# Optimization experiments

Hardware: AMD Instinct MI355X
Metric: run time of the kernel (lower is better)

## Reference

```python
import jax, jax.numpy as jnp
import numpy as np


def setup_inputs() -> dict:
    key = jax.random.key(0)
    k1, = jax.random.split(key, 1)
    b, l, h, w, c = 2, 16, 16, 16, 32
    inputs = jax.random.normal(k1, (b, l, h, w, c), dtype=jnp.float32)
    gamma = jnp.ones((1,), dtype=jnp.float32)
    return {"inputs": inputs, "gamma": gamma}


def reference(inputs, gamma):
    b, l, h, w, c = inputs.shape
    n = l * h * w
    # torch: x = permute->view gives [b, c, n]; here keep [b, n, c] (same memory layout of values)
    xr = inputs.reshape(b, n, c)
    # scores[b,i,j] = sum_c x[b,c,i] * x[b,c,j]
    scores = jnp.einsum('bic,bjc->bij', xr, xr)
    attn = jax.nn.softmax(scores, axis=-1)  # softmax over j (dim=-1)
    # out[b,c,j] = sum_i x[b,c,i] * attn[b,i,j]  ->  [b, n, c] layout
    out = jnp.einsum('bic,bij->bjc', xr, attn)
    out = out.reshape(b, l, h, w, c)
    return out * gamma + inputs
```

## Files before the change

### kernel.cpp

```cpp
#include <hip/hip_runtime.h>


typedef _Float16 half8 __attribute__((ext_vector_type(8)));
typedef _Float16 half4v __attribute__((ext_vector_type(4)));
typedef _Float16 half2v __attribute__((ext_vector_type(2)));
typedef float float4v __attribute__((ext_vector_type(4)));
typedef int int4v __attribute__((ext_vector_type(4)));

#define NN 4096
#define CC 32
#define L2E 1.44269504f
#define SHIFT 48.0f

__global__ __launch_bounds__(256) void k_convert(const float* __restrict__ x,
                                                 _Float16* __restrict__ xf,
                                                 _Float16* __restrict__ xt) {
    const int t = blockIdx.x * 256 + threadIdx.x;
    const int n  = t & 4095;
    const int cg = (t >> 12) & 7;
    const int b  = t >> 15;
    const int row = (b << 12) | n;
    const float4* src = (const float4*)(x + (size_t)row * CC + cg * 4);
    float4 v = *src;
    _Float16 h0 = (_Float16)v.x, h1 = (_Float16)v.y, h2 = (_Float16)v.z, h3 = (_Float16)v.w;
    *(half4v*)(xf + (size_t)row * CC + cg * 4) = (half4v){h0, h1, h2, h3};
    _Float16* xtb = xt + (size_t)b * CC * NN;
    xtb[(cg * 4 + 0) * NN + n] = h0;
    xtb[(cg * 4 + 1) * NN + n] = h1;
    xtb[(cg * 4 + 2) * NN + n] = h2;
    xtb[(cg * 4 + 3) * NN + n] = h3;
}

__global__ __launch_bounds__(512, 4) void k_pass1(const _Float16* __restrict__ xf,
                                                  float* __restrict__ c2out) {
    const int tid = threadIdx.x;
    const int wave = tid >> 6, lane = tid & 63;
    const int quad = lane >> 4, l15 = lane & 15;
    const int b = blockIdx.x >> 8;
    const int i0 = (blockIdx.x & 255) * 16;
    const _Float16* xb = xf + (size_t)b * NN * CC;

    const half8 afrag = *(const half8*)(xb + (size_t)(i0 + l15) * CC + quad * 8);
    const float4v zf = {0.f, 0.f, 0.f, 0.f};
    float z[4] = {0.f, 0.f, 0.f, 0.f};
    const float c2c = -SHIFT * L2E;

    const int jbase = wave * 512;
    half8 b0 = *(const half8*)(xb + (size_t)(jbase + l15) * CC + quad * 8);
    half8 b1 = *(const half8*)(xb + (size_t)(jbase + 16 + l15) * CC + quad * 8);
    half8 b2 = *(const half8*)(xb + (size_t)(jbase + 32 + l15) * CC + quad * 8);
    half8 b3 = *(const half8*)(xb + (size_t)(jbase + 48 + l15) * CC + quad * 8);

    for (int jt = 0; jt < 8; ++jt) {
        const int jn = jbase + ((jt + 1) & 7) * 64;
        half8 n0 = *(const half8*)(xb + (size_t)(jn + l15) * CC + quad * 8);
        half8 n1 = *(const half8*)(xb + (size_t)(jn + 16 + l15) * CC + quad * 8);
        half8 n2 = *(const half8*)(xb + (size_t)(jn + 32 + l15) * CC + quad * 8);
        half8 n3 = *(const half8*)(xb + (size_t)(jn + 48 + l15) * CC + quad * 8);

        float4v s0 = __builtin_amdgcn_mfma_f32_16x16x32_f16(afrag, b0, zf, 0, 0, 0);
        float4v s1 = __builtin_amdgcn_mfma_f32_16x16x32_f16(afrag, b1, zf, 0, 0, 0);
        float4v s2 = __builtin_amdgcn_mfma_f32_16x16x32_f16(afrag, b2, zf, 0, 0, 0);
        float4v s3 = __builtin_amdgcn_mfma_f32_16x16x32_f16(afrag, b3, zf, 0, 0, 0);
#pragma unroll
        for (int r = 0; r < 4; ++r) {
            z[r] += __builtin_amdgcn_exp2f(fmaf(s0[r], L2E, c2c));
            z[r] += __builtin_amdgcn_exp2f(fmaf(s1[r], L2E, c2c));
            z[r] += __builtin_amdgcn_exp2f(fmaf(s2[r], L2E, c2c));
            z[r] += __builtin_amdgcn_exp2f(fmaf(s3[r], L2E, c2c));
        }
        b0 = n0; b1 = n1; b2 = n2; b3 = n3;
    }
#pragma unroll
    for (int off = 1; off <= 8; off <<= 1) {
#pragma unroll
        for (int r = 0; r < 4; ++r) z[r] += __shfl_xor(z[r], off, 64);
    }
    __shared__ float zw[8][16];
    if (l15 == 0) {
#pragma unroll
        for (int r = 0; r < 4; ++r) zw[wave][quad * 4 + r] = z[r];
    }
    __syncthreads();
    if (tid < 16) {
        float zs = 0.f;
#pragma unroll
        for (int w = 0; w < 8; ++w) zs += zw[w][tid];
        c2out[b * NN + i0 + tid] = -(__builtin_amdgcn_logf(zs) + SHIFT * L2E);
    }
}

__global__ __launch_bounds__(512, 4) void k_pass2(const _Float16* __restrict__ xf,
                                                  const _Float16* __restrict__ xt,
                                                  const float* __restrict__ c2,
                                                  const float* __restrict__ x,
                                                  const float* __restrict__ gamma,
                                                  float* __restrict__ out) {
    const int tid = threadIdx.x;
    const int wave = tid >> 6, lane = tid & 63;
    const int quad = lane >> 4, l15 = lane & 15;
    const int b = blockIdx.x >> 8;
    const int j0 = (blockIdx.x & 255) * 16;
    const _Float16* xb  = xf + (size_t)b * NN * CC;
    const _Float16* xtb = xt + (size_t)b * CC * NN;
    const float* c2b = c2 + b * NN;

    __shared__ float red[8][16][32];

    const int addrLo = (((quad & 1) << 5) + l15) << 2;
    const int addrHi = addrLo + 64;
    const bool lo32 = (lane < 32);

    const half8 bjfrag = *(const half8*)(xb + (size_t)(j0 + l15) * CC + quad * 8);
    const float4v zf = {0.f, 0.f, 0.f, 0.f};
    float4v acc0 = zf, acc1 = zf;

    const int ibase = wave * 512;
    half8 a0  = *(const half8*)(xb + (size_t)(ibase + l15) * CC + quad * 8);
    half8 a1  = *(const half8*)(xb + (size_t)(ibase + 16 + l15) * CC + quad * 8);
    half8 xb0 = *(const half8*)(xtb + (size_t)l15 * NN + ibase + quad * 8);
    half8 xb1 = *(const half8*)(xtb + (size_t)(l15 + 16) * NN + ibase + quad * 8);
    float4v c20 = *(const float4v*)(c2b + ibase + quad * 4);
    float4v c21 = *(const float4v*)(c2b + ibase + 16 + quad * 4);

    for (int it = 0; it < 16; ++it) {
        const int inx = ibase + ((it + 1) & 15) * 32;
        half8 na0  = *(const half8*)(xb + (size_t)(inx + l15) * CC + quad * 8);
        half8 na1  = *(const half8*)(xb + (size_t)(inx + 16 + l15) * CC + quad * 8);
        half8 nxb0 = *(const half8*)(xtb + (size_t)l15 * NN + inx + quad * 8);
        half8 nxb1 = *(const half8*)(xtb + (size_t)(l15 + 16) * NN + inx + quad * 8);
        float4v nc20 = *(const float4v*)(c2b + inx + quad * 4);
        float4v nc21 = *(const float4v*)(c2b + inx + 16 + quad * 4);

        float4v s0 = __builtin_amdgcn_mfma_f32_16x16x32_f16(a0, bjfrag, zf, 0, 0, 0);
        float4v s1 = __builtin_amdgcn_mfma_f32_16x16x32_f16(a1, bjfrag, zf, 0, 0, 0);
        float4v e0, e1;
#pragma unroll
        for (int r = 0; r < 4; ++r) {
            e0[r] = __builtin_amdgcn_exp2f(fmaf(s0[r], L2E, c20[r]));
            e1[r] = __builtin_amdgcn_exp2f(fmaf(s1[r], L2E, c21[r]));
        }
        const int d0 = __builtin_bit_cast(int, (half2v)__builtin_amdgcn_cvt_pkrtz(e0[0], e0[1]));
        const int d1 = __builtin_bit_cast(int, (half2v)__builtin_amdgcn_cvt_pkrtz(e0[2], e0[3]));
        const int d2 = __builtin_bit_cast(int, (half2v)__builtin_amdgcn_cvt_pkrtz(e1[0], e1[1]));
        const int d3 = __builtin_bit_cast(int, (half2v)__builtin_amdgcn_cvt_pkrtz(e1[2], e1[3]));
        const int q0 = __builtin_amdgcn_ds_bpermute(addrLo, d0);
        const int q1 = __builtin_amdgcn_ds_bpermute(addrLo, d1);
        const int q2 = __builtin_amdgcn_ds_bpermute(addrHi, d0);
        const int q3 = __builtin_amdgcn_ds_bpermute(addrHi, d1);
        const int q4 = __builtin_amdgcn_ds_bpermute(addrLo, d2);
        const int q5 = __builtin_amdgcn_ds_bpermute(addrLo, d3);
        const int q6 = __builtin_amdgcn_ds_bpermute(addrHi, d2);
        const int q7 = __builtin_amdgcn_ds_bpermute(addrHi, d3);
        int4v ai;
        ai[0] = lo32 ? q0 : q4;
        ai[1] = lo32 ? q1 : q5;
        ai[2] = lo32 ? q2 : q6;
        ai[3] = lo32 ? q3 : q7;
        const half8 a2 = __builtin_bit_cast(half8, ai);

        acc0 = __builtin_amdgcn_mfma_f32_16x16x32_f16(a2, xb0, acc0, 0, 0, 0);
        acc1 = __builtin_amdgcn_mfma_f32_16x16x32_f16(a2, xb1, acc1, 0, 0, 0);

        a0 = na0; a1 = na1; xb0 = nxb0; xb1 = nxb1; c20 = nc20; c21 = nc21;
    }

#pragma unroll
    for (int r = 0; r < 4; ++r) {
        red[wave][quad * 4 + r][l15]      = acc0[r];
        red[wave][quad * 4 + r][l15 + 16] = acc1[r];
    }
    __syncthreads();
    {
        const int jj = tid >> 5, c = tid & 31;
        float s = 0.f;
#pragma unroll
        for (int w = 0; w < 8; ++w) s += red[w][jj][c];
        const float g = gamma[0];
        const size_t o = (size_t)(b * NN + j0 + jj) * CC + c;
        out[o] = fmaf(g, s, x[o]);
    }
}

extern "C" void kernel_launch(void* const* d_in, const int* in_sizes, int n_in,
                              void* d_out, int out_size, void* d_ws, size_t ws_size,
                              hipStream_t stream) {
    const float* x     = (const float*)d_in[0];
    const float* gamma = (const float*)d_in[1];
    float* out = (float*)d_out;

    _Float16* xf = (_Float16*)d_ws;
    _Float16* xt = xf + (size_t)2 * NN * CC;
    float*    c2 = (float*)(xt + (size_t)2 * CC * NN);

    k_convert<<<dim3(256), dim3(256), 0, stream>>>(x, xf, xt);
    k_pass1 <<<dim3(512), dim3(512), 0, stream>>>(xf, c2);
    k_pass2 <<<dim3(512), dim3(512), 0, stream>>>(xf, xt, c2, x, gamma, out);
}
```

Measured before the change: 93.24 us.

## Fuse convert, pass1 and pass2 into one cooperative kernel with grid syncs

Merges the three kernel launches into a single cooperative kernel that loops over tiles and separates the phases with grid-wide barriers. The goal is to remove launch overhead and inter-kernel gaps between the conversion, normalizer and output passes. In exchange it adds two grid.sync calls, host-side attribute and occupancy queries on every launch, and a grid capped by occupancy, which may mean fewer concurrent blocks per phase. The three-kernel path remains as a fallback.

```diff
diff --git a/kernel.cpp b/kernel.cpp
--- a/kernel.cpp
+++ b/kernel.cpp
@@ -1,5 +1,8 @@
 #include <hip/hip_runtime.h>
-
+#include <hip/hip_cooperative_groups.h>
+
+
+namespace cg = cooperative_groups;
 
 typedef _Float16 half8 __attribute__((ext_vector_type(8)));
 typedef _Float16 half4v __attribute__((ext_vector_type(4)));
@@ -12,32 +15,33 @@
 #define L2E 1.44269504f
 #define SHIFT 48.0f
 
-__global__ __launch_bounds__(256) void k_convert(const float* __restrict__ x,
-                                                 _Float16* __restrict__ xf,
-                                                 _Float16* __restrict__ xt) {
-    const int t = blockIdx.x * 256 + threadIdx.x;
+
+__device__ __forceinline__ void convert_body(int t, const float* __restrict__ x,
+                                             _Float16* __restrict__ xf,
+                                             _Float16* __restrict__ xt) {
     const int n  = t & 4095;
-    const int cg = (t >> 12) & 7;
+    const int cg_ = (t >> 12) & 7;
     const int b  = t >> 15;
     const int row = (b << 12) | n;
-    const float4* src = (const float4*)(x + (size_t)row * CC + cg * 4);
+    const float4* src = (const float4*)(x + (size_t)row * CC + cg_ * 4);
     float4 v = *src;
     _Float16 h0 = (_Float16)v.x, h1 = (_Float16)v.y, h2 = (_Float16)v.z, h3 = (_Float16)v.w;
-    *(half4v*)(xf + (size_t)row * CC + cg * 4) = (half4v){h0, h1, h2, h3};
+    *(half4v*)(xf + (size_t)row * CC + cg_ * 4) = (half4v){h0, h1, h2, h3};
     _Float16* xtb = xt + (size_t)b * CC * NN;
-    xtb[(cg * 4 + 0) * NN + n] = h0;
-    xtb[(cg * 4 + 1) * NN + n] = h1;
-    xtb[(cg * 4 + 2) * NN + n] = h2;
-    xtb[(cg * 4 + 3) * NN + n] = h3;
-}
-
-__global__ __launch_bounds__(512, 4) void k_pass1(const _Float16* __restrict__ xf,
-                                                  float* __restrict__ c2out) {
-    const int tid = threadIdx.x;
+    xtb[(cg_ * 4 + 0) * NN + n] = h0;
+    xtb[(cg_ * 4 + 1) * NN + n] = h1;
+    xtb[(cg_ * 4 + 2) * NN + n] = h2;
+    xtb[(cg_ * 4 + 3) * NN + n] = h3;
+}
+
+__device__ __forceinline__ void pass1_tile(int tile, int tid,
+                                           const _Float16* __restrict__ xf,
+                                           float* __restrict__ c2out,
+                                           float (*zw)[16]) {
     const int wave = tid >> 6, lane = tid & 63;
     const int quad = lane >> 4, l15 = lane & 15;
-    const int b = blockIdx.x >> 8;
-    const int i0 = (blockIdx.x & 255) * 16;
+    const int b = tile >> 8;
+    const int i0 = (tile & 255) * 16;
     const _Float16* xb = xf + (size_t)b * NN * CC;
 
     const half8 afrag = *(const half8*)(xb + (size_t)(i0 + l15) * CC + quad * 8);
@@ -76,7 +80,6 @@
 #pragma unroll
         for (int r = 0; r < 4; ++r) z[r] += __shfl_xor(z[r], off, 64);
     }
-    __shared__ float zw[8][16];
     if (l15 == 0) {
 #pragma unroll
         for (int r = 0; r < 4; ++r) zw[wave][quad * 4 + r] = z[r];
@@ -90,22 +93,21 @@
     }
 }
 
-__global__ __launch_bounds__(512, 4) void k_pass2(const _Float16* __restrict__ xf,
-                                                  const _Float16* __restrict__ xt,
-                                                  const float* __restrict__ c2,
-                                                  const float* __restrict__ x,
-                                                  const float* __restrict__ gamma,
-                                                  float* __restrict__ out) {
-    const int tid = threadIdx.x;
+__device__ __forceinline__ void pass2_tile(int tile, int tid,
+                                           const _Float16* __restrict__ xf,
+                                           const _Float16* __restrict__ xt,
+                                           const float* __restrict__ c2,
+                                           const float* __restrict__ x,
+                                           const float* __restrict__ gamma,
+                                           float* __restrict__ out,
+                                           float (*red)[16][32]) {
     const int wave = tid >> 6, lane = tid & 63;
     const int quad = lane >> 4, l15 = lane & 15;
-    const int b = blockIdx.x >> 8;
-    const int j0 = (blockIdx.x & 255) * 16;
+    const int b = tile >> 8;
+    const int j0 = (tile & 255) * 16;
     const _Float16* xb  = xf + (size_t)b * NN * CC;
     const _Float16* xtb = xt + (size_t)b * CC * NN;
     const float* c2b = c2 + b * NN;
-
-    __shared__ float red[8][16][32];
 
     const int addrLo = (((quad & 1) << 5) + l15) << 2;
     const int addrHi = addrLo + 64;
@@ -182,6 +184,60 @@
     }
 }
 
+
+__global__ __launch_bounds__(512, 4) void k_fused(const float* __restrict__ x,
+                                                  const float* __restrict__ gamma,
+                                                  _Float16* __restrict__ xf,
+                                                  _Float16* __restrict__ xt,
+                                                  float* __restrict__ c2,
+                                                  float* __restrict__ out) {
+    cg::grid_group grid = cg::this_grid();
+    const int tid = threadIdx.x;
+    const int nb = gridDim.x;
+
+    __shared__ float zw[8][16];
+    __shared__ float red[8][16][32];
+
+    for (int t = blockIdx.x * 512 + tid; t < 65536; t += nb * 512)
+        convert_body(t, x, xf, xt);
+    grid.sync();
+
+    for (int tile = blockIdx.x; tile < 512; tile += nb) {
+        pass1_tile(tile, tid, xf, c2, zw);
+        __syncthreads();
+    }
+    grid.sync();
+
+    for (int tile = blockIdx.x; tile < 512; tile += nb) {
+        pass2_tile(tile, tid, xf, xt, c2, x, gamma, out, red);
+        __syncthreads();
+    }
+}
+
+
+__global__ __launch_bounds__(256) void k_convert(const float* __restrict__ x,
+                                                 _Float16* __restrict__ xf,
+                                                 _Float16* __restrict__ xt) {
+    const int t = blockIdx.x * 256 + threadIdx.x;
+    convert_body(t, x, xf, xt);
+}
+
+__global__ __launch_bounds__(512, 4) void k_pass1(const _Float16* __restrict__ xf,
+                                                  float* __restrict__ c2out) {
+    __shared__ float zw[8][16];
+    pass1_tile(blockIdx.x, threadIdx.x, xf, c2out, zw);
+}
+
+__global__ __launch_bounds__(512, 4) void k_pass2(const _Float16* __restrict__ xf,
+                                                  const _Float16* __restrict__ xt,
+                                                  const float* __restrict__ c2,
+                                                  const float* __restrict__ x,
+                                                  const float* __restrict__ gamma,
+                                                  float* __restrict__ out) {
+    __shared__ float red[8][16][32];
+    pass2_tile(blockIdx.x, threadIdx.x, xf, xt, c2, x, gamma, out, red);
+}
+
 extern "C" void kernel_launch(void* const* d_in, const int* in_sizes, int n_in,
                               void* d_out, int out_size, void* d_ws, size_t ws_size,
                               hipStream_t stream) {
@@ -193,6 +249,20 @@
     _Float16* xt = xf + (size_t)2 * NN * CC;
     float*    c2 = (float*)(xt + (size_t)2 * CC * NN);
 
+    int coopAttr = 0;
+    (void)hipDeviceGetAttribute(&coopAttr, hipDeviceAttributeCooperativeLaunch, 0);
+    int occ = 0;
+    hipError_t oe = hipOccupancyMaxActiveBlocksPerMultiprocessor(&occ, k_fused, 512, 0);
+
+    if (coopAttr && oe == hipSuccess && occ > 0) {
+        int grid = occ * 256;
+        if (grid > 512) grid = 512;
+        void* args[] = {(void*)&x, (void*)&gamma, (void*)&xf, (void*)&xt, (void*)&c2, (void*)&out};
+        hipError_t le = hipLaunchCooperativeKernel(k_fused, dim3(grid), dim3(512),
+                                                   args, 0u, stream);
+        if (le == hipSuccess) return;
+    }
+
     k_convert<<<dim3(256), dim3(256), 0, stream>>>(x, xf, xt);
     k_pass1 <<<dim3(512), dim3(512), 0, stream>>>(xf, c2);
     k_pass2 <<<dim3(512), dim3(512), 0, stream>>>(xf, xt, c2, x, gamma, out);
```

Result: slower. 175.6 us (+88.3%).

## Process 32 query rows per block to reuse streamed key/value fragments

Applied to the files above, without the earlier changes.

Each block of both passes now handles 32 rows instead of 16, so each loaded j (or i) fragment feeds twice as many MFMAs. This halves redundant global/L2 traffic for streamed operands and the grid size. The trade-off is more registers per thread (launch bounds lowered to 2 blocks per CU), more shared memory for the reduction, and only 256 blocks, which may underfill the 256 CUs of the device.

```diff
diff --git a/kernel.cpp b/kernel.cpp
--- a/kernel.cpp
+++ b/kernel.cpp
@@ -31,18 +31,20 @@
     xtb[(cg * 4 + 3) * NN + n] = h3;
 }
 
-__global__ __launch_bounds__(512, 4) void k_pass1(const _Float16* __restrict__ xf,
+__global__ __launch_bounds__(512, 2) void k_pass1(const _Float16* __restrict__ xf,
                                                   float* __restrict__ c2out) {
     const int tid = threadIdx.x;
     const int wave = tid >> 6, lane = tid & 63;
     const int quad = lane >> 4, l15 = lane & 15;
-    const int b = blockIdx.x >> 8;
-    const int i0 = (blockIdx.x & 255) * 16;
+    const int b = blockIdx.x >> 7;
+    const int i0 = (blockIdx.x & 127) * 32;
     const _Float16* xb = xf + (size_t)b * NN * CC;
 
-    const half8 afrag = *(const half8*)(xb + (size_t)(i0 + l15) * CC + quad * 8);
+    const half8 af0 = *(const half8*)(xb + (size_t)(i0 + l15) * CC + quad * 8);
+    const half8 af1 = *(const half8*)(xb + (size_t)(i0 + 16 + l15) * CC + quad * 8);
     const float4v zf = {0.f, 0.f, 0.f, 0.f};
-    float z[4] = {0.f, 0.f, 0.f, 0.f};
+    float z0[4] = {0.f, 0.f, 0.f, 0.f};
+    float z1[4] = {0.f, 0.f, 0.f, 0.f};
     const float c2c = -SHIFT * L2E;
 
     const int jbase = wave * 512;
@@ -58,31 +60,45 @@
         half8 n2 = *(const half8*)(xb + (size_t)(jn + 32 + l15) * CC + quad * 8);
         half8 n3 = *(const half8*)(xb + (size_t)(jn + 48 + l15) * CC + quad * 8);
 
-        float4v s0 = __builtin_amdgcn_mfma_f32_16x16x32_f16(afrag, b0, zf, 0, 0, 0);
-        float4v s1 = __builtin_amdgcn_mfma_f32_16x16x32_f16(afrag, b1, zf, 0, 0, 0);
-        float4v s2 = __builtin_amdgcn_mfma_f32_16x16x32_f16(afrag, b2, zf, 0, 0, 0);
-        float4v s3 = __builtin_amdgcn_mfma_f32_16x16x32_f16(afrag, b3, zf, 0, 0, 0);
-#pragma unroll
-        for (int r = 0; r < 4; ++r) {
-            z[r] += __builtin_amdgcn_exp2f(fmaf(s0[r], L2E, c2c));
-            z[r] += __builtin_amdgcn_exp2f(fmaf(s1[r], L2E, c2c));
-            z[r] += __builtin_amdgcn_exp2f(fmaf(s2[r], L2E, c2c));
-            z[r] += __builtin_amdgcn_exp2f(fmaf(s3[r], L2E, c2c));
+        float4v s00 = __builtin_amdgcn_mfma_f32_16x16x32_f16(af0, b0, zf, 0, 0, 0);
+        float4v s01 = __builtin_amdgcn_mfma_f32_16x16x32_f16(af0, b1, zf, 0, 0, 0);
+        float4v s02 = __builtin_amdgcn_mfma_f32_16x16x32_f16(af0, b2, zf, 0, 0, 0);
+        float4v s03 = __builtin_amdgcn_mfma_f32_16x16x32_f16(af0, b3, zf, 0, 0, 0);
+        float4v s10 = __builtin_amdgcn_mfma_f32_16x16x32_f16(af1, b0, zf, 0, 0, 0);
+        float4v s11 = __builtin_amdgcn_mfma_f32_16x16x32_f16(af1, b1, zf, 0, 0, 0);
+        float4v s12 = __builtin_amdgcn_mfma_f32_16x16x32_f16(af1, b2, zf, 0, 0, 0);
+        float4v s13 = __builtin_amdgcn_mfma_f32_16x16x32_f16(af1, b3, zf, 0, 0, 0);
+#pragma unroll
+        for (int r = 0; r < 4; ++r) {
+            z0[r] += __builtin_amdgcn_exp2f(fmaf(s00[r], L2E, c2c));
+            z0[r] += __builtin_amdgcn_exp2f(fmaf(s01[r], L2E, c2c));
+            z0[r] += __builtin_amdgcn_exp2f(fmaf(s02[r], L2E, c2c));
+            z0[r] += __builtin_amdgcn_exp2f(fmaf(s03[r], L2E, c2c));
+            z1[r] += __builtin_amdgcn_exp2f(fmaf(s10[r], L2E, c2c));
+            z1[r] += __builtin_amdgcn_exp2f(fmaf(s11[r], L2E, c2c));
+            z1[r] += __builtin_amdgcn_exp2f(fmaf(s12[r], L2E, c2c));
+            z1[r] += __builtin_amdgcn_exp2f(fmaf(s13[r], L2E, c2c));
         }
         b0 = n0; b1 = n1; b2 = n2; b3 = n3;
     }
 #pragma unroll
     for (int off = 1; off <= 8; off <<= 1) {
 #pragma unroll
-        for (int r = 0; r < 4; ++r) z[r] += __shfl_xor(z[r], off, 64);
-    }
-    __shared__ float zw[8][16];
+        for (int r = 0; r < 4; ++r) {
+            z0[r] += __shfl_xor(z0[r], off, 64);
+            z1[r] += __shfl_xor(z1[r], off, 64);
+        }
+    }
+    __shared__ float zw[8][32];
     if (l15 == 0) {
 #pragma unroll
-        for (int r = 0; r < 4; ++r) zw[wave][quad * 4 + r] = z[r];
+        for (int r = 0; r < 4; ++r) {
+            zw[wave][quad * 4 + r]      = z0[r];
+            zw[wave][16 + quad * 4 + r] = z1[r];
+        }
     }
     __syncthreads();
-    if (tid < 16) {
+    if (tid < 32) {
         float zs = 0.f;
 #pragma unroll
         for (int w = 0; w < 8; ++w) zs += zw[w][tid];
@@ -90,7 +106,7 @@
     }
 }
 
-__global__ __launch_bounds__(512, 4) void k_pass2(const _Float16* __restrict__ xf,
+__global__ __launch_bounds__(512, 2) void k_pass2(const _Float16* __restrict__ xf,
                                                   const _Float16* __restrict__ xt,
                                                   const float* __restrict__ c2,
                                                   const float* __restrict__ x,
@@ -99,21 +115,22 @@
     const int tid = threadIdx.x;
     const int wave = tid >> 6, lane = tid & 63;
     const int quad = lane >> 4, l15 = lane & 15;
-    const int b = blockIdx.x >> 8;
-    const int j0 = (blockIdx.x & 255) * 16;
+    const int b = blockIdx.x >> 7;
+    const int j0 = (blockIdx.x & 127) * 32;
     const _Float16* xb  = xf + (size_t)b * NN * CC;
     const _Float16* xtb = xt + (size_t)b * CC * NN;
     const float* c2b = c2 + b * NN;
 
-    __shared__ float red[8][16][32];
+    __shared__ float red[8][32][32];
 
     const int addrLo = (((quad & 1) << 5) + l15) << 2;
     const int addrHi = addrLo + 64;
     const bool lo32 = (lane < 32);
 
-    const half8 bjfrag = *(const half8*)(xb + (size_t)(j0 + l15) * CC + quad * 8);
+    const half8 bj0 = *(const half8*)(xb + (size_t)(j0 + l15) * CC + quad * 8);
+    const half8 bj1 = *(const half8*)(xb + (size_t)(j0 + 16 + l15) * CC + quad * 8);
     const float4v zf = {0.f, 0.f, 0.f, 0.f};
-    float4v acc0 = zf, acc1 = zf;
+    float4v acc00 = zf, acc01 = zf, acc10 = zf, acc11 = zf;
 
     const int ibase = wave * 512;
     half8 a0  = *(const half8*)(xb + (size_t)(ibase + l15) * CC + quad * 8);
@@ -132,53 +149,86 @@
         float4v nc20 = *(const float4v*)(c2b + inx + quad * 4);
         float4v nc21 = *(const float4v*)(c2b + inx + 16 + quad * 4);
 
-        float4v s0 = __builtin_amdgcn_mfma_f32_16x16x32_f16(a0, bjfrag, zf, 0, 0, 0);
-        float4v s1 = __builtin_amdgcn_mfma_f32_16x16x32_f16(a1, bjfrag, zf, 0, 0, 0);
-        float4v e0, e1;
-#pragma unroll
-        for (int r = 0; r < 4; ++r) {
-            e0[r] = __builtin_amdgcn_exp2f(fmaf(s0[r], L2E, c20[r]));
-            e1[r] = __builtin_amdgcn_exp2f(fmaf(s1[r], L2E, c21[r]));
-        }
-        const int d0 = __builtin_bit_cast(int, (half2v)__builtin_amdgcn_cvt_pkrtz(e0[0], e0[1]));
-        const int d1 = __builtin_bit_cast(int, (half2v)__builtin_amdgcn_cvt_pkrtz(e0[2], e0[3]));
-        const int d2 = __builtin_bit_cast(int, (half2v)__builtin_amdgcn_cvt_pkrtz(e1[0], e1[1]));
-        const int d3 = __builtin_bit_cast(int, (half2v)__builtin_amdgcn_cvt_pkrtz(e1[2], e1[3]));
-        const int q0 = __builtin_amdgcn_ds_bpermute(addrLo, d0);
-        const int q1 = __builtin_amdgcn_ds_bpermute(addrLo, d1);
-        const int q2 = __builtin_amdgcn_ds_bpermute(addrHi, d0);
-        const int q3 = __builtin_amdgcn_ds_bpermute(addrHi, d1);
-        const int q4 = __builtin_amdgcn_ds_bpermute(addrLo, d2);
-        const int q5 = __builtin_amdgcn_ds_bpermute(addrLo, d3);
-        const int q6 = __builtin_amdgcn_ds_bpermute(addrHi, d2);
-        const int q7 = __builtin_amdgcn_ds_bpermute(addrHi, d3);
-        int4v ai;
-        ai[0] = lo32 ? q0 : q4;
-        ai[1] = lo32 ? q1 : q5;
-        ai[2] = lo32 ? q2 : q6;
-        ai[3] = lo32 ? q3 : q7;
-        const half8 a2 = __builtin_bit_cast(half8, ai);
-
-        acc0 = __builtin_amdgcn_mfma_f32_16x16x32_f16(a2, xb0, acc0, 0, 0, 0);
-        acc1 = __builtin_amdgcn_mfma_f32_16x16x32_f16(a2, xb1, acc1, 0, 0, 0);
+        float4v s00 = __builtin_amdgcn_mfma_f32_16x16x32_f16(a0, bj0, zf, 0, 0, 0);
+        float4v s10 = __builtin_amdgcn_mfma_f32_16x16x32_f16(a1, bj0, zf, 0, 0, 0);
+        float4v s01 = __builtin_amdgcn_mfma_f32_16x16x32_f16(a0, bj1, zf, 0, 0, 0);
+        float4v s11 = __builtin_amdgcn_mfma_f32_16x16x32_f16(a1, bj1, zf, 0, 0, 0);
+        float4v e00, e10, e01, e11;
+#pragma unroll
+        for (int r = 0; r < 4; ++r) {
+            e00[r] = __builtin_amdgcn_exp2f(fmaf(s00[r], L2E, c20[r]));
+            e10[r] = __builtin_amdgcn_exp2f(fmaf(s10[r], L2E, c21[r]));
+            e01[r] = __builtin_amdgcn_exp2f(fmaf(s01[r], L2E, c20[r]));
+            e11[r] = __builtin_amdgcn_exp2f(fmaf(s11[r], L2E, c21[r]));
+        }
+        {
+            const int d0 = __builtin_bit_cast(int, (half2v)__builtin_amdgcn_cvt_pkrtz(e00[0], e00[1]));
+            const int d1 = __builtin_bit_cast(int, (half2v)__builtin_amdgcn_cvt_pkrtz(e00[2], e00[3]));
+            const int d2 = __builtin_bit_cast(int, (half2v)__builtin_amdgcn_cvt_pkrtz(e10[0], e10[1]));
+            const int d3 = __builtin_bit_cast(int, (half2v)__builtin_amdgcn_cvt_pkrtz(e10[2], e10[3]));
+            const int q0 = __builtin_amdgcn_ds_bpermute(addrLo, d0);
+            const int q1 = __builtin_amdgcn_ds_bpermute(addrLo, d1);
+            const int q2 = __builtin_amdgcn_ds_bpermute(addrHi, d0);
+            const int q3 = __builtin_amdgcn_ds_bpermute(addrHi, d1);
+            const int q4 = __builtin_amdgcn_ds_bpermute(addrLo, d2);
+            const int q5 = __builtin_amdgcn_ds_bpermute(addrLo, d3);
+            const int q6 = __builtin_amdgcn_ds_bpermute(addrHi, d2);
+            const int q7 = __builtin_amdgcn_ds_bpermute(addrHi, d3);
+            int4v ai;
+            ai[0] = lo32 ? q0 : q4;
+            ai[1] = lo32 ? q1 : q5;
+            ai[2] = lo32 ? q2 : q6;
+            ai[3] = lo32 ? q3 : q7;
+            const half8 a2 = __builtin_bit_cast(half8, ai);
+            acc00 = __builtin_amdgcn_mfma_f32_16x16x32_f16(a2, xb0, acc00, 0, 0, 0);
+            acc01 = __builtin_amdgcn_mfma_f32_16x16x32_f16(a2, xb1, acc01, 0, 0, 0);
+        }
+        {
+            const int d0 = __builtin_bit_cast(int, (half2v)__builtin_amdgcn_cvt_pkrtz(e01[0], e01[1]));
+            const int d1 = __builtin_bit_cast(int, (half2v)__builtin_amdgcn_cvt_pkrtz(e01[2], e01[3]));
+            const int d2 = __builtin_bit_cast(int, (half2v)__builtin_amdgcn_cvt_pkrtz(e11[0], e11[1]));
+            const int d3 = __builtin_bit_cast(int, (half2v)__builtin_amdgcn_cvt_pkrtz(e11[2], e11[3]));
+            const int q0 = __builtin_amdgcn_ds_bpermute(addrLo, d0);
+            const int q1 = __builtin_amdgcn_ds_bpermute(addrLo, d1);
+            const int q2 = __builtin_amdgcn_ds_bpermute(addrHi, d0);
+            const int q3 = __builtin_amdgcn_ds_bpermute(addrHi, d1);
+            const int q4 = __builtin_amdgcn_ds_bpermute(addrLo, d2);
+            const int q5 = __builtin_amdgcn_ds_bpermute(addrLo, d3);
+            const int q6 = __builtin_amdgcn_ds_bpermute(addrHi, d2);
+            const int q7 = __builtin_amdgcn_ds_bpermute(addrHi, d3);
+            int4v ai;
+            ai[0] = lo32 ? q0 : q4;
+            ai[1] = lo32 ? q1 : q5;
+            ai[2] = lo32 ? q2 : q6;
+            ai[3] = lo32 ? q3 : q7;
+            const half8 a2 = __builtin_bit_cast(half8, ai);
+            acc10 = __builtin_amdgcn_mfma_f32_16x16x32_f16(a2, xb0, acc10, 0, 0, 0);
+            acc11 = __builtin_amdgcn_mfma_f32_16x16x32_f16(a2, xb1, acc11, 0, 0, 0);
+        }
 
         a0 = na0; a1 = na1; xb0 = nxb0; xb1 = nxb1; c20 = nc20; c21 = nc21;
     }
 
 #pragma unroll
     for (int r = 0; r < 4; ++r) {
-        red[wave][quad * 4 + r][l15]      = acc0[r];
-        red[wave][quad * 4 + r][l15 + 16] = acc1[r];
+        red[wave][quad * 4 + r][l15]           = acc00[r];
+        red[wave][quad * 4 + r][l15 + 16]      = acc01[r];
+        red[wave][16 + quad * 4 + r][l15]      = acc10[r];
+        red[wave][16 + quad * 4 + r][l15 + 16] = acc11[r];
     }
     __syncthreads();
     {
         const int jj = tid >> 5, c = tid & 31;
-        float s = 0.f;
-#pragma unroll
-        for (int w = 0; w < 8; ++w) s += red[w][jj][c];
         const float g = gamma[0];
-        const size_t o = (size_t)(b * NN + j0 + jj) * CC + c;
-        out[o] = fmaf(g, s, x[o]);
+#pragma unroll
+        for (int h = 0; h < 2; ++h) {
+            const int j = jj + h * 16;
+            float s = 0.f;
+#pragma unroll
+            for (int w = 0; w < 8; ++w) s += red[w][j][c];
+            const size_t o = (size_t)(b * NN + j0 + j) * CC + c;
+            out[o] = fmaf(g, s, x[o]);
+        }
     }
 }
 
@@ -194,6 +244,6 @@
     float*    c2 = (float*)(xt + (size_t)2 * CC * NN);
 
     k_convert<<<dim3(256), dim3(256), 0, stream>>>(x, xf, xt);
-    k_pass1 <<<dim3(512), dim3(512), 0, stream>>>(xf, c2);
-    k_pass2 <<<dim3(512), dim3(512), 0, stream>>>(xf, xt, c2, x, gamma, out);
-}
+    k_pass1 <<<dim3(256), dim3(512), 0, stream>>>(xf, c2);
+    k_pass2 <<<dim3(256), dim3(512), 0, stream>>>(xf, xt, c2, x, gamma, out);
+}
```

New measurement: 79.65 us. 1.17x faster.
